# Kernel optimization log

Measured on AMD Instinct MI355X. Metric: run time of the kernel, lower is better.

Reference implementation:

```python
import jax, jax.numpy as jnp
import numpy as np

N_EXPERTS = 16
IN_DIM = 1024
OUT_DIM = 1024
BATCH = 4096

def setup_inputs() -> dict:
    key = jax.random.key(0)
    k1, k2, k3, k4 = jax.random.split(key, 4)
    x = jax.random.normal(k1, (BATCH, IN_DIM), dtype=jnp.float32)
    comp_weight = jax.random.uniform(k2, (BATCH, N_EXPERTS), dtype=jnp.float32)
    # torch.rand init (uniform [0,1)) per original module
    weight = jax.random.uniform(k3, (N_EXPERTS, IN_DIM, OUT_DIM), dtype=jnp.float32)
    bias = jax.random.uniform(k4, (N_EXPERTS, OUT_DIM), dtype=jnp.float32)
    return {"x": x, "comp_weight": comp_weight, "weight": weight, "bias": bias}

def reference(x, comp_weight, weight, bias):
    # z[n,b,o] = x[b,i] @ weight[n,i,o] + bias[n,o]   (baddbmm)
    z = jnp.einsum('bi,nio->nbo', x, weight) + bias[:, None, :]
    # out[b,o] = sum_n comp_weight[b,n] * z[n,b,o]    (bmm combine)
    out = jnp.einsum('bn,nbo->bo', comp_weight, z)
    return jax.nn.relu(out)
```

## Files before the change

kernel.cpp:

```cpp
#include <hip/hip_runtime.h>
#include <hip/hip_bf16.h>
#include <cstdint>

#define BATCH   4096
#define IN_DIM  1024
#define OUT_DIM 1024
#define NEXP    16

typedef __bf16 bf16;
typedef __attribute__((ext_vector_type(8))) __bf16 bf16x8;
typedef __attribute__((ext_vector_type(4))) float  f32x4;

#define AS1 __attribute__((address_space(1)))
#define AS3 __attribute__((address_space(3)))

__device__ __forceinline__ void gld_lds16(const bf16* g, bf16* l) {
    __builtin_amdgcn_global_load_lds((const AS1 void*)g, (AS3 void*)l, 16, 0, 0);
}

__global__ void convert_x_tiled(const float* __restrict__ x, bf16* __restrict__ xt) {
    int tile = blockIdx.x;
    int mblk = tile >> 4, ks = tile & 15;
    int t = threadIdx.x;
#pragma unroll
    for (int r = 0; r < 4; r++) {
        int q = r * 256 + t;
        int m_loc = q >> 3, sc = q & 7;
        int c = sc ^ (m_loc & 7);
        const float* src = x + (size_t)(mblk * 128 + m_loc) * IN_DIM + ks * 64 + c * 8;
        f32x4 a = *(const f32x4*)src;
        f32x4 b = *(const f32x4*)(src + 4);
        bf16x8 v;
#pragma unroll
        for (int j = 0; j < 4; j++) { v[j] = (bf16)a[j]; v[4 + j] = (bf16)b[j]; }
        *(bf16x8*)(xt + (size_t)tile * 8192 + q * 8) = v;
    }
}

__global__ void convert_w_frag(const float* __restrict__ W, bf16* __restrict__ wt) {
    int tile = blockIdx.x;
    int nblk = tile >> 8, ne = (tile >> 4) & 15, ks = tile & 15;
    int t = threadIdx.x;
#pragma unroll
    for (int r = 0; r < 2; r++) {
        int c = r * 256 + t;
        int sub = c >> 6, l = c & 63;
        int lr = l & 15, lq = l >> 4;
        int kk = sub >> 2, wn = (sub >> 1) & 1, nt = sub & 1;
        int kbase = ne * 1024 + ks * 64 + kk * 32 + lq * 8;
        int ng = nblk * 64 + wn * 32 + nt * 16 + lr;
        bf16x8 v;
#pragma unroll
        for (int j = 0; j < 8; j++)
            v[j] = (bf16)W[(size_t)(kbase + j) * OUT_DIM + ng];
        *(bf16x8*)(wt + (size_t)tile * 4096 + c * 8) = v;
    }
}

__global__ __launch_bounds__(256, 3) void moe_gemm(
        const float* __restrict__ cw, const float* __restrict__ bias,
        const bf16* __restrict__ xt, const bf16* __restrict__ wt,
        float* __restrict__ out) {
    int nblk = blockIdx.x;
    int mblk = blockIdx.y;
    int m0 = mblk * 128, n0 = nblk * 64;
    int t = threadIdx.x;
    int lane = t & 63, w = t >> 6;
    int wm = w >> 1, wn = w & 1;
    int lq = lane >> 4, lr = lane & 15;

    __shared__ bf16 As[128 * 64];
    __shared__ bf16 Bs[2][64 * 64];
    __shared__ float cwT[16 * 132];

#pragma unroll
    for (int r = 0; r < 2; r++) {
        int q = r * 256 + t;
        f32x4 v = *(const f32x4*)(cw + (size_t)m0 * NEXP + q * 4);
        int row = q >> 2, nb = (q & 3) * 4;
#pragma unroll
        for (int c2 = 0; c2 < 4; c2++) cwT[(nb + c2) * 132 + row] = v[c2];
    }

    const f32x4 fz = {0.f, 0.f, 0.f, 0.f};
    f32x4 acc[4][2];
#pragma unroll
    for (int mt = 0; mt < 4; mt++)
#pragma unroll
        for (int nt = 0; nt < 2; nt++) acc[mt][nt] = fz;

    int swz = lr & 7;
    int mrow[4];
#pragma unroll
    for (int mt = 0; mt < 4; mt++) mrow[mt] = (wm * 64 + mt * 16 + lr) * 64;

    const bf16* abase = xt + (size_t)(mblk * 16) * 8192;
    const bf16* bbase = wt + (size_t)nblk * (16 * 16 * 4096);

    for (int ks = 0; ks < 16; ks++) {
        const bf16* asrc = abase + (size_t)ks * 8192 + t * 8;
#pragma unroll
        for (int r = 0; r < 4; r++) gld_lds16(asrc + r * 2048, &As[r * 2048 + t * 8]);
        const bf16* b0 = bbase + (size_t)ks * 4096 + t * 8;
#pragma unroll
        for (int r = 0; r < 2; r++) gld_lds16(b0 + r * 2048, &Bs[0][r * 2048 + t * 8]);
        __syncthreads();

        bf16x8 af[4][2];
#pragma unroll
        for (int kk = 0; kk < 2; kk++)
#pragma unroll
            for (int mt = 0; mt < 4; mt++)
                af[mt][kk] = *(const bf16x8*)&As[mrow[mt] + ((kk * 4 + lq) ^ swz) * 8];

#pragma unroll 2
        for (int ne = 0; ne < NEXP; ne++) {
            int buf = ne & 1;
            if (ne < 15) {
                const bf16* bn = bbase + (size_t)((ne + 1) * 16 + ks) * 4096 + t * 8;
#pragma unroll
                for (int r = 0; r < 2; r++)
                    gld_lds16(bn + r * 2048, &Bs[buf ^ 1][r * 2048 + t * 8]);
            }
            bf16x8 bfr[2][2];
#pragma unroll
            for (int kk = 0; kk < 2; kk++)
#pragma unroll
                for (int nt = 0; nt < 2; nt++)
                    bfr[kk][nt] = *(const bf16x8*)
                        &Bs[buf][((kk * 2 + wn) * 2 + nt) * 512 + lane * 8];
            f32x4 s[4];
#pragma unroll
            for (int mt = 0; mt < 4; mt++)
                s[mt] = *(const f32x4*)&cwT[ne * 132 + wm * 64 + mt * 16 + lq * 4];
#pragma unroll
            for (int mt = 0; mt < 4; mt++)
#pragma unroll
                for (int nt = 0; nt < 2; nt++) {
                    f32x4 p = __builtin_amdgcn_mfma_f32_16x16x32_bf16(
                        af[mt][0], bfr[0][nt], fz, 0, 0, 0);
                    p = __builtin_amdgcn_mfma_f32_16x16x32_bf16(
                        af[mt][1], bfr[1][nt], p, 0, 0, 0);
                    acc[mt][nt] += s[mt] * p;
                }
            __syncthreads();
        }
    }

    {
        bf16x8 acw[4];
#pragma unroll
        for (int mt = 0; mt < 4; mt++) {
            bf16x8 v;
#pragma unroll
            for (int j = 0; j < 8; j++) v[j] = (bf16)0.f;
            if (lq < 2) {
                int row = m0 + wm * 64 + mt * 16 + lr;
                f32x4 a = *(const f32x4*)(cw + (size_t)row * NEXP + lq * 8);
                f32x4 b = *(const f32x4*)(cw + (size_t)row * NEXP + lq * 8 + 4);
#pragma unroll
                for (int j = 0; j < 4; j++) { v[j] = (bf16)a[j]; v[4 + j] = (bf16)b[j]; }
            }
            acw[mt] = v;
        }
        bf16x8 bb[2];
#pragma unroll
        for (int nt = 0; nt < 2; nt++) {
            bf16x8 v;
#pragma unroll
            for (int j = 0; j < 8; j++) v[j] = (bf16)0.f;
            if (lq < 2) {
                int col = n0 + wn * 32 + nt * 16 + lr;
#pragma unroll
                for (int j = 0; j < 8; j++)
                    v[j] = (bf16)bias[(size_t)(lq * 8 + j) * OUT_DIM + col];
            }
            bb[nt] = v;
        }
#pragma unroll
        for (int mt = 0; mt < 4; mt++)
#pragma unroll
            for (int nt = 0; nt < 2; nt++)
                acc[mt][nt] = __builtin_amdgcn_mfma_f32_16x16x32_bf16(
                    acw[mt], bb[nt], acc[mt][nt], 0, 0, 0);
    }

#pragma unroll
    for (int mt = 0; mt < 4; mt++) {
        int row = m0 + wm * 64 + mt * 16 + lq * 4;
#pragma unroll
        for (int nt = 0; nt < 2; nt++) {
            int col = n0 + wn * 32 + nt * 16 + lr;
#pragma unroll
            for (int r2 = 0; r2 < 4; r2++) {
                float v = acc[mt][nt][r2];
                out[(size_t)(row + r2) * OUT_DIM + col] = v > 0.f ? v : 0.f;
            }
        }
    }
}

__global__ void fallback_kernel(const float* __restrict__ x, const float* __restrict__ cw,
                                const float* __restrict__ W, const float* __restrict__ bias,
                                float* __restrict__ out) {
    int o = blockIdx.x * 256 + threadIdx.x;
    int b = o >> 10, oc = o & 1023;
    const float* xr = x + (size_t)b * IN_DIM;
    float accv = 0.f;
    for (int n = 0; n < NEXP; n++) {
        const float* wr = W + (size_t)n * IN_DIM * OUT_DIM + oc;
        float z = 0.f;
        for (int i = 0; i < IN_DIM; i++) z += xr[i] * wr[(size_t)i * OUT_DIM];
        accv += cw[(size_t)b * NEXP + n] * (z + bias[n * OUT_DIM + oc]);
    }
    out[o] = accv > 0.f ? accv : 0.f;
}

extern "C" void kernel_launch(void* const* d_in, const int* in_sizes, int n_in,
                              void* d_out, int out_size, void* d_ws, size_t ws_size,
                              hipStream_t stream) {
    const float* x    = (const float*)d_in[0];
    const float* cw   = (const float*)d_in[1];
    const float* W    = (const float*)d_in[2];
    const float* bias = (const float*)d_in[3];
    float* out = (float*)d_out;

    const size_t wt_elems = (size_t)NEXP * IN_DIM * OUT_DIM;
    const size_t xt_elems = (size_t)BATCH * IN_DIM;
    if (ws_size < (wt_elems + xt_elems) * sizeof(bf16)) {
        fallback_kernel<<<(BATCH * OUT_DIM) / 256, 256, 0, stream>>>(x, cw, W, bias, out);
        return;
    }
    bf16* wt = (bf16*)d_ws;
    bf16* xt = wt + wt_elems;

    convert_w_frag<<<4096, 256, 0, stream>>>(W, wt);
    convert_x_tiled<<<512, 256, 0, stream>>>(x, xt);
    moe_gemm<<<dim3(16, 32), 256, 0, stream>>>(cw, bias, xt, wt, out);
}
```

Baseline: 256.3 us.

## Merge conversion kernels with LDS-transposed W and deepen GEMM prefetch pipeline

Merges the W and x conversion kernels into one launch. The W conversion now stages a coalesced 64x64 tile through shared memory before writing the fragment layout, replacing strided scalar global reads. The GEMM double-buffers A, uses a four-deep B ring prefetched two experts ahead, and replaces full __syncthreads with explicit vmcnt waits plus raw barriers and s_setprio around the MFMAs. The larger LDS footprint lowers the occupancy target from three to two blocks per CU, and the hand-counted waits are fragile if the load counts change.

```diff
diff --git a/kernel.cpp b/kernel.cpp
--- a/kernel.cpp
+++ b/kernel.cpp
@@ -18,46 +18,63 @@
     __builtin_amdgcn_global_load_lds((const AS1 void*)g, (AS3 void*)l, 16, 0, 0);
 }
 
-__global__ void convert_x_tiled(const float* __restrict__ x, bf16* __restrict__ xt) {
-    int tile = blockIdx.x;
-    int mblk = tile >> 4, ks = tile & 15;
+__device__ __forceinline__ void wait_vm0() { asm volatile("s_waitcnt vmcnt(0)" ::: "memory"); }
+__device__ __forceinline__ void wait_vm2() { asm volatile("s_waitcnt vmcnt(2)" ::: "memory"); }
+__device__ __forceinline__ void wait_vm4() { asm volatile("s_waitcnt vmcnt(4)" ::: "memory"); }
+__device__ __forceinline__ void wait_vm8() { asm volatile("s_waitcnt vmcnt(8)" ::: "memory"); }
+
+__global__ __launch_bounds__(256) void convert_all(
+        const float* __restrict__ x, const float* __restrict__ W,
+        bf16* __restrict__ xt, bf16* __restrict__ wt) {
+    __shared__ float Ls[64][65];
     int t = threadIdx.x;
-#pragma unroll
-    for (int r = 0; r < 4; r++) {
-        int q = r * 256 + t;
-        int m_loc = q >> 3, sc = q & 7;
-        int c = sc ^ (m_loc & 7);
-        const float* src = x + (size_t)(mblk * 128 + m_loc) * IN_DIM + ks * 64 + c * 8;
-        f32x4 a = *(const f32x4*)src;
-        f32x4 b = *(const f32x4*)(src + 4);
-        bf16x8 v;
-#pragma unroll
-        for (int j = 0; j < 4; j++) { v[j] = (bf16)a[j]; v[4 + j] = (bf16)b[j]; }
-        *(bf16x8*)(xt + (size_t)tile * 8192 + q * 8) = v;
-    }
-}
-
-__global__ void convert_w_frag(const float* __restrict__ W, bf16* __restrict__ wt) {
-    int tile = blockIdx.x;
-    int nblk = tile >> 8, ne = (tile >> 4) & 15, ks = tile & 15;
-    int t = threadIdx.x;
-#pragma unroll
-    for (int r = 0; r < 2; r++) {
-        int c = r * 256 + t;
-        int sub = c >> 6, l = c & 63;
-        int lr = l & 15, lq = l >> 4;
-        int kk = sub >> 2, wn = (sub >> 1) & 1, nt = sub & 1;
-        int kbase = ne * 1024 + ks * 64 + kk * 32 + lq * 8;
-        int ng = nblk * 64 + wn * 32 + nt * 16 + lr;
-        bf16x8 v;
-#pragma unroll
-        for (int j = 0; j < 8; j++)
-            v[j] = (bf16)W[(size_t)(kbase + j) * OUT_DIM + ng];
-        *(bf16x8*)(wt + (size_t)tile * 4096 + c * 8) = v;
-    }
-}
-
-__global__ __launch_bounds__(256, 3) void moe_gemm(
+    int bid = blockIdx.x;
+    if (bid < 4096) {
+        int nblk = bid >> 8, ne = (bid >> 4) & 15, ks = bid & 15;
+        int kb = ne * 1024 + ks * 64;
+        int n0 = nblk * 64;
+#pragma unroll
+        for (int r = 0; r < 4; r++) {
+            int idx = r * 256 + t;
+            int row = idx >> 4, c4 = (idx & 15) * 4;
+            f32x4 v = *(const f32x4*)(W + (size_t)(kb + row) * OUT_DIM + n0 + c4);
+#pragma unroll
+            for (int j = 0; j < 4; j++) Ls[row][c4 + j] = v[j];
+        }
+        __syncthreads();
+#pragma unroll
+        for (int r = 0; r < 2; r++) {
+            int c = r * 256 + t;
+            int sub = c >> 6, l = c & 63;
+            int lr = l & 15, lq = l >> 4;
+            int kk = sub >> 2, wn = (sub >> 1) & 1, nt = sub & 1;
+            int krow = kk * 32 + lq * 8;
+            int col = wn * 32 + nt * 16 + lr;
+            bf16x8 v;
+#pragma unroll
+            for (int j = 0; j < 8; j++) v[j] = (bf16)Ls[krow + j][col];
+            *(bf16x8*)(wt + (size_t)bid * 4096 + c * 8) = v;
+        }
+    } else {
+        int tile = bid - 4096;
+        int mblk = tile >> 4, ks = tile & 15;
+#pragma unroll
+        for (int r = 0; r < 4; r++) {
+            int q = r * 256 + t;
+            int m_loc = q >> 3, sc = q & 7;
+            int cc = sc ^ (m_loc & 7);
+            const float* src = x + (size_t)(mblk * 128 + m_loc) * IN_DIM + ks * 64 + cc * 8;
+            f32x4 a = *(const f32x4*)src;
+            f32x4 b = *(const f32x4*)(src + 4);
+            bf16x8 v;
+#pragma unroll
+            for (int j = 0; j < 4; j++) { v[j] = (bf16)a[j]; v[4 + j] = (bf16)b[j]; }
+            *(bf16x8*)(xt + (size_t)tile * 8192 + q * 8) = v;
+        }
+    }
+}
+
+__global__ __launch_bounds__(256, 2) void moe_gemm(
         const float* __restrict__ cw, const float* __restrict__ bias,
         const bf16* __restrict__ xt, const bf16* __restrict__ wt,
         float* __restrict__ out) {
@@ -69,8 +86,8 @@
     int wm = w >> 1, wn = w & 1;
     int lq = lane >> 4, lr = lane & 15;
 
-    __shared__ bf16 As[128 * 64];
-    __shared__ bf16 Bs[2][64 * 64];
+    __shared__ bf16 As[2][128 * 64];
+    __shared__ bf16 Bs[4][64 * 64];
     __shared__ float cwT[16 * 132];
 
 #pragma unroll
@@ -81,6 +98,22 @@
 #pragma unroll
         for (int c2 = 0; c2 < 4; c2++) cwT[(nb + c2) * 132 + row] = v[c2];
     }
+    __syncthreads();
+
+    const bf16* abase = xt + (size_t)(mblk * 16) * 8192;
+    const bf16* bbase = wt + (size_t)nblk * (16 * 16 * 4096);
+
+    {
+        const bf16* a0 = abase + t * 8;
+#pragma unroll
+        for (int r = 0; r < 4; r++) gld_lds16(a0 + r * 2048, &As[0][r * 2048 + t * 8]);
+        const bf16* b0 = bbase + t * 8;
+#pragma unroll
+        for (int r = 0; r < 2; r++) gld_lds16(b0 + r * 2048, &Bs[0][r * 2048 + t * 8]);
+        const bf16* b1 = bbase + (size_t)16 * 4096 + t * 8;
+#pragma unroll
+        for (int r = 0; r < 2; r++) gld_lds16(b1 + r * 2048, &Bs[1][r * 2048 + t * 8]);
+    }
 
     const f32x4 fz = {0.f, 0.f, 0.f, 0.f};
     f32x4 acc[4][2];
@@ -94,58 +127,71 @@
 #pragma unroll
     for (int mt = 0; mt < 4; mt++) mrow[mt] = (wm * 64 + mt * 16 + lr) * 64;
 
-    const bf16* abase = xt + (size_t)(mblk * 16) * 8192;
-    const bf16* bbase = wt + (size_t)nblk * (16 * 16 * 4096);
-
-    for (int ks = 0; ks < 16; ks++) {
-        const bf16* asrc = abase + (size_t)ks * 8192 + t * 8;
-#pragma unroll
-        for (int r = 0; r < 4; r++) gld_lds16(asrc + r * 2048, &As[r * 2048 + t * 8]);
-        const bf16* b0 = bbase + (size_t)ks * 4096 + t * 8;
-#pragma unroll
-        for (int r = 0; r < 2; r++) gld_lds16(b0 + r * 2048, &Bs[0][r * 2048 + t * 8]);
-        __syncthreads();
-
-        bf16x8 af[4][2];
+    bf16x8 af[4][2];
+
+    auto step = [&](int ne, int ks, bool stage_b, bool stage_a, int wsel) {
+        if (stage_b) {
+            int ks2 = ks + ((ne + 2) >> 4);
+            int ne2 = (ne + 2) & 15;
+            const bf16* bn = bbase + (size_t)(ne2 * 16 + ks2) * 4096 + t * 8;
+            bf16* dst = &Bs[(ne + 2) & 3][t * 8];
+#pragma unroll
+            for (int r = 0; r < 2; r++) gld_lds16(bn + r * 2048, dst + r * 2048);
+        }
+        if (stage_a) {
+            const bf16* an = abase + (size_t)(ks + 1) * 8192 + t * 8;
+            bf16* dst = &As[(ks + 1) & 1][t * 8];
+#pragma unroll
+            for (int r = 0; r < 4; r++) gld_lds16(an + r * 2048, dst + r * 2048);
+        }
+        if (wsel == 0) wait_vm4();
+        else if (wsel == 1) wait_vm8();
+        else if (wsel == 2) wait_vm2();
+        else wait_vm0();
+        __builtin_amdgcn_s_barrier();
+        asm volatile("" ::: "memory");
+
+        if (ne == 0) {
+#pragma unroll
+            for (int kk = 0; kk < 2; kk++)
+#pragma unroll
+                for (int mt = 0; mt < 4; mt++)
+                    af[mt][kk] = *(const bf16x8*)
+                        &As[ks & 1][mrow[mt] + ((kk * 4 + lq) ^ swz) * 8];
+        }
+        bf16x8 bfr[2][2];
 #pragma unroll
         for (int kk = 0; kk < 2; kk++)
 #pragma unroll
-            for (int mt = 0; mt < 4; mt++)
-                af[mt][kk] = *(const bf16x8*)&As[mrow[mt] + ((kk * 4 + lq) ^ swz) * 8];
-
-#pragma unroll 2
-        for (int ne = 0; ne < NEXP; ne++) {
-            int buf = ne & 1;
-            if (ne < 15) {
-                const bf16* bn = bbase + (size_t)((ne + 1) * 16 + ks) * 4096 + t * 8;
-#pragma unroll
-                for (int r = 0; r < 2; r++)
-                    gld_lds16(bn + r * 2048, &Bs[buf ^ 1][r * 2048 + t * 8]);
-            }
-            bf16x8 bfr[2][2];
-#pragma unroll
-            for (int kk = 0; kk < 2; kk++)
-#pragma unroll
-                for (int nt = 0; nt < 2; nt++)
-                    bfr[kk][nt] = *(const bf16x8*)
-                        &Bs[buf][((kk * 2 + wn) * 2 + nt) * 512 + lane * 8];
-            f32x4 s[4];
-#pragma unroll
-            for (int mt = 0; mt < 4; mt++)
-                s[mt] = *(const f32x4*)&cwT[ne * 132 + wm * 64 + mt * 16 + lq * 4];
-#pragma unroll
-            for (int mt = 0; mt < 4; mt++)
-#pragma unroll
-                for (int nt = 0; nt < 2; nt++) {
-                    f32x4 p = __builtin_amdgcn_mfma_f32_16x16x32_bf16(
-                        af[mt][0], bfr[0][nt], fz, 0, 0, 0);
-                    p = __builtin_amdgcn_mfma_f32_16x16x32_bf16(
-                        af[mt][1], bfr[1][nt], p, 0, 0, 0);
-                    acc[mt][nt] += s[mt] * p;
-                }
-            __syncthreads();
-        }
-    }
+            for (int nt = 0; nt < 2; nt++)
+                bfr[kk][nt] = *(const bf16x8*)
+                    &Bs[ne & 3][((kk * 2 + wn) * 2 + nt) * 512 + lane * 8];
+        f32x4 s[4];
+#pragma unroll
+        for (int mt = 0; mt < 4; mt++)
+            s[mt] = *(const f32x4*)&cwT[ne * 132 + wm * 64 + mt * 16 + lq * 4];
+        __builtin_amdgcn_s_setprio(1);
+#pragma unroll
+        for (int mt = 0; mt < 4; mt++)
+#pragma unroll
+            for (int nt = 0; nt < 2; nt++) {
+                f32x4 p = __builtin_amdgcn_mfma_f32_16x16x32_bf16(
+                    af[mt][0], bfr[0][nt], fz, 0, 0, 0);
+                p = __builtin_amdgcn_mfma_f32_16x16x32_bf16(
+                    af[mt][1], bfr[1][nt], p, 0, 0, 0);
+                acc[mt][nt] += s[mt] * p;
+            }
+        __builtin_amdgcn_s_setprio(0);
+    };
+
+    for (int ks = 0; ks < 15; ks++) {
+#pragma unroll
+        for (int ne = 0; ne < 16; ne++)
+            step(ne, ks, true, ne == 13, (ne >= 13) ? 1 : 0);
+    }
+#pragma unroll
+    for (int ne = 0; ne < 16; ne++)
+        step(ne, 15, ne <= 13, false, ne <= 13 ? 0 : (ne == 14 ? 2 : 3));
 
     {
         bf16x8 acw[4];
@@ -234,7 +280,6 @@
     bf16* wt = (bf16*)d_ws;
     bf16* xt = wt + wt_elems;
 
-    convert_w_frag<<<4096, 256, 0, stream>>>(W, wt);
-    convert_x_tiled<<<512, 256, 0, stream>>>(x, xt);
+    convert_all<<<4096 + 512, 256, 0, stream>>>(x, W, xt, wt);
     moe_gemm<<<dim3(16, 32), 256, 0, stream>>>(cw, bias, xt, wt, out);
 }
```

New measurement: 392.5 us. 1.53x slower.
